# Kernel optimization log

Hardware: AMD Instinct MI355X
Metric: run time of the kernel (lower is better)

## Reference

```python
import jax, jax.numpy as jnp
import numpy as np

FIELD_DIMS = [26000] * 39
EMBED_DIM = 16
MLP_DIMS = [1024, 512, 256]
BATCH = 16384
EPS = 1e-5
OFFSETS = jnp.asarray(np.concatenate(([0], np.cumsum(FIELD_DIMS)[:-1])), dtype=jnp.int64)


def _bn_fields(x, g, b):
    # BatchNorm1d(num_fields) on (B, F, E): stats over (batch, embed) per field (training-mode batch stats)
    mu = x.mean(axis=(0, 2), keepdims=True)
    var = x.var(axis=(0, 2), keepdims=True)
    return (x - mu) / jnp.sqrt(var + EPS) * g[None, :, None] + b[None, :, None]


def _bn1d(x, g, b):
    # BatchNorm1d on (B, D): stats over batch
    mu = x.mean(axis=0)
    var = x.var(axis=0)
    return (x - mu) / jnp.sqrt(var + EPS) * g + b


def setup_inputs() -> dict:
    key = jax.random.key(0)
    ks = jax.random.split(key, 16)
    V = sum(FIELD_DIMS)
    F = len(FIELD_DIMS)
    E = EMBED_DIM
    D = F * E  # 624
    init = lambda k, shape, s: (jax.random.normal(k, shape) * s).astype(jnp.float32)
    inp = {}
    inp["x"] = jax.random.randint(ks[0], (BATCH, F), 0, FIELD_DIMS[0], dtype=jnp.int64)
    inp["emb_table"] = init(ks[1], (V, E), 0.01)
    inp["lin_table"] = init(ks[2], (V, 1), 0.01)
    inp["lin_bias"] = jnp.zeros((1,), jnp.float32)
    inp["bn_g"] = jnp.ones((F,), jnp.float32)
    inp["bn_b"] = jnp.zeros((F,), jnp.float32)
    inp["ctrl_w"] = init(ks[3], (D, F), D ** -0.5)
    inp["ctrl_b"] = jnp.zeros((F,), jnp.float32)
    inp["ctrl_bn_g"] = jnp.ones((F,), jnp.float32)
    inp["ctrl_bn_b"] = jnp.zeros((F,), jnp.float32)
    dims = [D] + MLP_DIMS
    for i in range(3):
        inp[f"w{i+1}"] = init(ks[4 + i], (dims[i], dims[i + 1]), dims[i] ** -0.5)
        inp[f"b{i+1}"] = jnp.zeros((dims[i + 1],), jnp.float32)
        inp[f"g{i+1}"] = jnp.ones((dims[i + 1],), jnp.float32)
        inp[f"be{i+1}"] = jnp.zeros((dims[i + 1],), jnp.float32)
    inp["w_out"] = init(ks[7], (dims[-1], 1), dims[-1] ** -0.5)
    inp["b_out"] = jnp.zeros((1,), jnp.float32)
    inp["k"] = 20
    return inp


def reference(x, emb_table, lin_table, lin_bias, bn_g, bn_b,
              ctrl_w, ctrl_b, ctrl_bn_g, ctrl_bn_b,
              w1, b1, g1, be1, w2, b2, g2, be2, w3, b3, g3, be3,
              w_out, b_out, k):
    B, F = x.shape
    idx = x + OFFSETS[None, :]                      # (B, F) global vocab ids
    embed = emb_table[idx]                          # (B, F, E) gather
    embed = _bn_fields(embed, bn_g, bn_b)
    flat = embed.reshape(B, -1)                     # (B, F*E)
    # controller MLP: Linear -> BN -> ReLU (dropout inactive at inference)
    weight = jax.nn.relu(_bn1d(flat @ ctrl_w + ctrl_b, ctrl_bn_g, ctrl_bn_b))  # (B, F)
    # kmax_pooling along dim 1: topk values, indices sorted ascending
    kvals, kidx = jax.lax.top_k(weight, k)          # (B, k)
    order = jnp.argsort(kidx, axis=1)
    kidx = jnp.take_along_axis(kidx, order, axis=1)
    kvals = jnp.take_along_axis(kvals, order, axis=1)
    kvals = kvals / jnp.sum(kvals, axis=1, keepdims=True)
    # scatter normalized weights into zero mask
    mask = jnp.zeros((B, F), embed.dtype).at[jnp.arange(B)[:, None], kidx].set(kvals)
    embed = embed * mask[:, :, None]                # elementwise gate
    # wide part: sum of per-field scalar embeddings + bias
    linear = lin_table[idx].sum(axis=1) + lin_bias  # (B, 1)
    # deep part: 3-layer MLP with BN+ReLU, final Linear to 1
    h = embed.reshape(B, -1)
    h = jax.nn.relu(_bn1d(h @ w1 + b1, g1, be1))
    h = jax.nn.relu(_bn1d(h @ w2 + b2, g2, be2))
    h = jax.nn.relu(_bn1d(h @ w3 + b3, g3, be3))
    out = linear + h @ w_out + b_out                # (B, 1)
    return jax.nn.sigmoid(out.squeeze(1))           # (B,)
```

## Files before the change

kernel.cpp:

```cpp
#include <hip/hip_runtime.h>
#include <math.h>
#include <stdint.h>

constexpr int BB = 16384;
constexpr int NF = 39;
constexpr int NE = 16;
constexpr int ND = NF * NE;
constexpr int FIELD_DIM = 26000;
constexpr float EPS_ = 1e-5f;

typedef __bf16 bfx8 __attribute__((ext_vector_type(8)));
typedef float f32x4 __attribute__((ext_vector_type(4)));
typedef short s16x8 __attribute__((ext_vector_type(8)));

static __device__ __forceinline__ unsigned short f2bf(float f) {
    union { float f; unsigned u; } a; a.f = f;
    unsigned r = a.u + 0x7fffu + ((a.u >> 16) & 1u);
    return (unsigned short)(r >> 16);
}
static __device__ __forceinline__ float bf2f(unsigned short u) {
    union { unsigned u; float f; } a; a.u = ((unsigned)u) << 16;
    return a.f;
}

static __device__ __forceinline__ void xcd_map(int l, int lognx, int& bx, int& by) {
    int s = l >> 3;
    bx = s & ((1 << lognx) - 1);
    by = ((l & 7) << 4) + (s >> lognx);
}

__global__ void k_prep(const float* __restrict__ w1, const float* __restrict__ w2,
                       const float* __restrict__ w3, const float* __restrict__ cw,
                       unsigned short* __restrict__ w1t, unsigned short* __restrict__ w2t,
                       unsigned short* __restrict__ w3t, float* __restrict__ wct,
                       double* __restrict__ stats, int nstats) {
    int b = blockIdx.x;
    if (b < 1280) {
        const float* in; unsigned short* outp; int K, N, Kpad, tid;
        if (b < 640)        { in = w1; outp = w1t; K = 624;  N = 1024; Kpad = 640;  tid = b; }
        else if (b < 1152)  { in = w2; outp = w2t; K = 1024; N = 512;  Kpad = 1024; tid = b - 640; }
        else                { in = w3; outp = w3t; K = 512;  N = 256;  Kpad = 512;  tid = b - 1152; }
        int tiles_n = N >> 5;
        int tk = tid / tiles_n, tn = tid % tiles_n;
        __shared__ float tile[32][33];
        int tx = threadIdx.x & 31, ty = threadIdx.x >> 5;
#pragma unroll
        for (int i = 0; i < 4; ++i) {
            int k = tk * 32 + ty + i * 8, n = tn * 32 + tx;
            tile[ty + i * 8][tx] = (k < K) ? in[(size_t)k * N + n] : 0.f;
        }
        __syncthreads();
#pragma unroll
        for (int i = 0; i < 4; ++i) {
            int n = tn * 32 + ty + i * 8, k = tk * 32 + tx;
            outp[(size_t)n * Kpad + k] = f2bf(tile[tx][ty + i * 8]);
        }
    } else if (b < 1397) {
        int gid = (b - 1280) * 256 + threadIdx.x;
        if (gid < 48 * ND) {
            int j = gid / ND, k = gid % ND;
            wct[gid] = (j < NF) ? cw[(size_t)k * NF + j] : 0.f;
        }
    } else {
        int gid = (b - 1397) * 256 + threadIdx.x;
        if (gid < nstats) stats[gid] = 0.0;
    }
}

__global__ void k_field_stats(const int* __restrict__ x, const float* __restrict__ emb,
                              double* __restrict__ stats ) {
    int f = blockIdx.x;
    int r = blockIdx.y * blockDim.x + threadIdx.x;
    double s = 0.0, q = 0.0;
    if (r < BB) {
        long long id = (long long)x[r * NF + f] + (long long)f * FIELD_DIM;
        const float4* p = (const float4*)(emb + id * NE);
#pragma unroll
        for (int i = 0; i < 4; ++i) {
            float4 v = p[i];
            s += (double)v.x; s += (double)v.y; s += (double)v.z; s += (double)v.w;
            q += (double)v.x * v.x; q += (double)v.y * v.y;
            q += (double)v.z * v.z; q += (double)v.w * v.w;
        }
    }
    __shared__ double ls[256], lq[256];
    ls[threadIdx.x] = s; lq[threadIdx.x] = q;
    __syncthreads();
    for (int off = 128; off > 0; off >>= 1) {
        if ((int)threadIdx.x < off) {
            ls[threadIdx.x] += ls[threadIdx.x + off];
            lq[threadIdx.x] += lq[threadIdx.x + off];
        }
        __syncthreads();
    }
    if (threadIdx.x == 0) {
        atomicAdd(&stats[f], ls[0]);
        atomicAdd(&stats[NF + f], lq[0]);
    }
}

__global__ void k_flat_norm(const int* __restrict__ x, const float* __restrict__ emb,
                            const double* __restrict__ stats, const float* __restrict__ bng,
                            const float* __restrict__ bnb, float* __restrict__ flat) {
    __shared__ float sc_s[NF], sh_s[NF];
    if ((int)threadIdx.x < NF) {
        int f = threadIdx.x;
        double cnt = (double)BB * NE;
        double mu = stats[f] / cnt;
        double var = stats[NF + f] / cnt - mu * mu;
        float sc = (float)((double)bng[f] / sqrt(var + (double)EPS_));
        sc_s[f] = sc;
        sh_s[f] = bnb[f] - (float)mu * sc;
    }
    __syncthreads();
    int gid = blockIdx.x * blockDim.x + threadIdx.x;
    if (gid >= BB * NF) return;
    int f = gid % NF;
    long long id = (long long)x[gid] + (long long)f * FIELD_DIM;
    float sc = sc_s[f], sh = sh_s[f];
    const float4* p = (const float4*)(emb + id * NE);
    float4* o = (float4*)(flat) + (size_t)gid * 4;
#pragma unroll
    for (int i = 0; i < 4; ++i) {
        float4 v = p[i];
        o[i] = make_float4(fmaf(v.x, sc, sh), fmaf(v.y, sc, sh),
                           fmaf(v.z, sc, sh), fmaf(v.w, sc, sh));
    }
}

__launch_bounds__(256)
__global__ void k_ctrl_gemm_sk(const float* __restrict__ flat, const float* __restrict__ wct,
                               double* __restrict__ zp) {
    __shared__ float As[64][68];
    __shared__ float Ws[64][49];
    const int t = threadIdx.x;
    const int tn = t & 15;
    const int tm = t >> 4;
    const int bm = blockIdx.x & 255;
    const int half = blockIdx.x >> 8;
    const int m0 = bm * 64;
    const int kbeg = half ? 320 : 0;
    const int kend = half ? 624 : 320;
    double acc[4][3] = {};
    for (int k0 = kbeg; k0 < kend; k0 += 64) {
        const int kl = (kend - k0 >= 64) ? 64 : (kend - k0);
        const int kl4 = kl >> 2;
#pragma unroll
        for (int i = 0; i < 4; ++i) {
            int idx = t + 256 * i;
            int row = idx >> 4, c4 = idx & 15;
            if (c4 < kl4) {
                float4 v = *(const float4*)(flat + (size_t)(m0 + row) * ND + k0 + c4 * 4);
                *(float4*)&As[row][c4 * 4] = v;
            }
        }
        {
            int col = t >> 4;
            int c4 = t & 15;
#pragma unroll
            for (int cp = 0; cp < 3; ++cp, col += 16) {
                if (c4 < kl4) {
                    float4 v = *(const float4*)(wct + (size_t)col * ND + k0 + c4 * 4);
                    Ws[c4 * 4 + 0][col] = v.x; Ws[c4 * 4 + 1][col] = v.y;
                    Ws[c4 * 4 + 2][col] = v.z; Ws[c4 * 4 + 3][col] = v.w;
                }
            }
        }
        __syncthreads();
#pragma unroll 4
        for (int kk = 0; kk < kl; ++kk) {
            double a0 = (double)As[4 * tm + 0][kk];
            double a1 = (double)As[4 * tm + 1][kk];
            double a2 = (double)As[4 * tm + 2][kk];
            double a3 = (double)As[4 * tm + 3][kk];
            double w0 = (double)Ws[kk][3 * tn + 0];
            double w1 = (double)Ws[kk][3 * tn + 1];
            double w2 = (double)Ws[kk][3 * tn + 2];
            acc[0][0] += a0 * w0; acc[0][1] += a0 * w1; acc[0][2] += a0 * w2;
            acc[1][0] += a1 * w0; acc[1][1] += a1 * w1; acc[1][2] += a1 * w2;
            acc[2][0] += a2 * w0; acc[2][1] += a2 * w1; acc[2][2] += a2 * w2;
            acc[3][0] += a3 * w0; acc[3][1] += a3 * w1; acc[3][2] += a3 * w2;
        }
        __syncthreads();
    }
    double* zph = zp + (size_t)half * BB * NF;
#pragma unroll
    for (int j = 0; j < 3; ++j) {
        int col = 3 * tn + j;
        if (col < NF) {
#pragma unroll
            for (int i = 0; i < 4; ++i)
                zph[(size_t)(m0 + 4 * tm + i) * NF + col] = acc[i][j];
        }
    }
}

__global__ void k_ctrl_reduce(const double* __restrict__ zp, const float* __restrict__ bias,
                              float* __restrict__ z, double* __restrict__ stats) {
    __shared__ double Sred[2][16][48];
    const int t = threadIdx.x;
    const int tn = t & 15;
    const int tm = t >> 4;
    const int m0 = blockIdx.x * 64;
#pragma unroll
    for (int j = 0; j < 3; ++j) {
        int col = 3 * tn + j;
        double s = 0.0, q = 0.0;
        if (col < NF) {
            float bs = bias[col];
#pragma unroll
            for (int i = 0; i < 4; ++i) {
                size_t idx = (size_t)(m0 + 4 * tm + i) * NF + col;
                double p01 = zp[idx] + zp[(size_t)BB * NF + idx];
                float v = (float)(p01 + (double)bs);
                z[idx] = v;
                s += (double)v;
                q += (double)v * (double)v;
            }
        }
        Sred[0][tm][col] = s;
        Sred[1][tm][col] = q;
    }
    __syncthreads();
    if (t < NF) {
        double ts = 0.0, tq = 0.0;
#pragma unroll
        for (int i = 0; i < 16; ++i) { ts += Sred[0][i][t]; tq += Sred[1][i][t]; }
        atomicAdd(&stats[t], ts);
        atomicAdd(&stats[NF + t], tq);
    }
}

__global__ void k_topk_gate(const float* __restrict__ zc, const double* __restrict__ stats,
                            const float* __restrict__ cbg, const float* __restrict__ cbb,
                            const int* __restrict__ kptr, const float* __restrict__ flat,
                            unsigned short* __restrict__ flatg) {
    __shared__ float sc_s[NF], sh_s[NF];
    int t = threadIdx.x;
    if (t < NF) {
        double mu = stats[t] / (double)BB;
        double var = stats[NF + t] / (double)BB - mu * mu;
        float sc = (float)((double)cbg[t] / sqrt(var + (double)EPS_));
        sc_s[t] = sc;
        sh_s[t] = cbb[t] - (float)mu * sc;
    }
    __syncthreads();
    int r = blockIdx.x * 4 + (t >> 6);
    int lane = t & 63;
    int k = kptr[0];
    bool active = (lane < NF);
    float w = -1.f;
    if (active) {
        float v = zc[(size_t)r * NF + lane];
        w = fmaxf(fmaf(v, sc_s[lane], sh_s[lane]), 0.f);
    }
    int rank = 0;
#pragma unroll
    for (int j = 0; j < NF; ++j) {
        float vj = __shfl(w, j, 64);
        rank += (vj > w || (vj == w && j < lane)) ? 1 : 0;
    }
    bool sel = active && (rank < k);
    float val = sel ? w : 0.f;
    float sum = val;
#pragma unroll
    for (int off = 32; off > 0; off >>= 1) sum += __shfl_xor(sum, off, 64);
    if (active) {
        float ms = sel ? ((sum > 0.f) ? (w / sum) : 0.f) : 0.f;
        const float* src = flat + (size_t)r * ND + lane * 16;
        unsigned short* dst = flatg + (size_t)r * 640 + lane * 16;
#pragma unroll
        for (int h = 0; h < 2; ++h) {
            union { s16x8 v; unsigned short u[8]; } p;
#pragma unroll
            for (int j = 0; j < 8; ++j) p.u[j] = f2bf(src[h * 8 + j] * ms);
            *(s16x8*)(dst + h * 8) = p.v;
        }
    } else if (lane == NF) {
        s16x8 zv = {};
        *(s16x8*)(flatg + (size_t)r * 640 + 624) = zv;
        *(s16x8*)(flatg + (size_t)r * 640 + 632) = zv;
    }
}

__launch_bounds__(256)
__global__ void k_mfma_gemm(const unsigned short* __restrict__ A,
                            const unsigned short* __restrict__ Bt,
                            const float* __restrict__ bias,
                            unsigned short* __restrict__ C,
                            double* __restrict__ stats,
                            int M, int K, int N, int lognx) {
    __shared__ char lds[65536];
    const int t = threadIdx.x;
    const int l = t & 63;
    const int w = t >> 6;
    int bx, by;
    xcd_map(blockIdx.x, lognx, bx, by);
    const int m0 = by * 128, n0 = bx * 128;
    const int Wr = (w >> 1) * 64, Wc = (w & 1) * 64;

    const int srow = t >> 3;
    const int sswz = (t & 7) ^ (srow & 7);
    const unsigned short* ga[4];
    const unsigned short* gb[4];
#pragma unroll
    for (int i = 0; i < 4; ++i) {
        ga[i] = A + (size_t)(m0 + i * 32 + srow) * K + sswz * 8;
        gb[i] = Bt + (size_t)(n0 + i * 32 + srow) * K + sswz * 8;
    }
    int a_off[4][2], b_off[4][2];
#pragma unroll
    for (int m = 0; m < 4; ++m) {
#pragma unroll
        for (int h = 0; h < 2; ++h) {
            int r = Wr + m * 16 + (l & 15);
            a_off[m][h] = r * 128 + (((h * 4 + (l >> 4)) ^ (r & 7)) << 4);
            int c = Wc + m * 16 + (l & 15);
            b_off[m][h] = c * 128 + (((h * 4 + (l >> 4)) ^ (c & 7)) << 4);
        }
    }
    const int nt = K >> 6;
    f32x4 acc[4][4] = {};
#pragma unroll
    for (int i = 0; i < 4; ++i) {
        __builtin_amdgcn_global_load_lds(
            (const __attribute__((address_space(1))) void*)ga[i],
            (__attribute__((address_space(3))) void*)(lds + i * 4096 + t * 16), 16, 0, 0);
        __builtin_amdgcn_global_load_lds(
            (const __attribute__((address_space(1))) void*)gb[i],
            (__attribute__((address_space(3))) void*)(lds + 32768 + i * 4096 + t * 16), 16, 0, 0);
        ga[i] += 64; gb[i] += 64;
    }
    __syncthreads();
    for (int ts = 0; ts < nt; ++ts) {
        const int cur = ts & 1;
        if (ts + 1 < nt) {
            char* An = lds + (cur ^ 1) * 16384;
            char* Bn = lds + 32768 + (cur ^ 1) * 16384;
#pragma unroll
            for (int i = 0; i < 4; ++i) {
                __builtin_amdgcn_global_load_lds(
                    (const __attribute__((address_space(1))) void*)ga[i],
                    (__attribute__((address_space(3))) void*)(An + i * 4096 + t * 16), 16, 0, 0);
                __builtin_amdgcn_global_load_lds(
                    (const __attribute__((address_space(1))) void*)gb[i],
                    (__attribute__((address_space(3))) void*)(Bn + i * 4096 + t * 16), 16, 0, 0);
                ga[i] += 64; gb[i] += 64;
            }
        }
        const char* Ac = lds + cur * 16384;
        const char* Bc = lds + 32768 + cur * 16384;
#pragma unroll
        for (int h = 0; h < 2; ++h) {
            bfx8 af[4], bv[4];
#pragma unroll
            for (int m = 0; m < 4; ++m)
                af[m] = __builtin_bit_cast(bfx8, *(const s16x8*)(Ac + a_off[m][h]));
#pragma unroll
            for (int n = 0; n < 4; ++n)
                bv[n] = __builtin_bit_cast(bfx8, *(const s16x8*)(Bc + b_off[n][h]));
#pragma unroll
            for (int m = 0; m < 4; ++m)
#pragma unroll
                for (int n = 0; n < 4; ++n)
                    acc[m][n] = __builtin_amdgcn_mfma_f32_16x16x32_bf16(af[m], bv[n], acc[m][n], 0, 0, 0);
        }
        __syncthreads();
    }
#pragma unroll
    for (int n = 0; n < 4; ++n) {
        int nc = n0 + Wc + n * 16 + (l & 15);
        float bs = bias[nc];
        double s = 0.0, q = 0.0;
#pragma unroll
        for (int m = 0; m < 4; ++m) {
            int rbase = m0 + Wr + m * 16 + ((l >> 4) << 2);
#pragma unroll
            for (int i = 0; i < 4; ++i) {
                float v = acc[m][n][i] + bs;
                C[(size_t)(rbase + i) * N + nc] = f2bf(v);
                s += (double)v;
                q += (double)v * (double)v;
            }
        }
        s += __shfl_xor(s, 16, 64); s += __shfl_xor(s, 32, 64);
        q += __shfl_xor(q, 16, 64); q += __shfl_xor(q, 32, 64);
        if ((l >> 4) == 0) {
            atomicAdd(&stats[nc], s);
            atomicAdd(&stats[N + nc], q);
        }
    }
}

__launch_bounds__(256)
__global__ void k_mfma_gemm_bn(const unsigned short* __restrict__ A,
                               const double* __restrict__ statsIn,
                               const float* __restrict__ g, const float* __restrict__ be,
                               const unsigned short* __restrict__ Bt,
                               const float* __restrict__ bias,
                               unsigned short* __restrict__ C,
                               double* __restrict__ stats,
                               int M, int K, int N, int lognx) {
    __shared__ char lds[73728];
    float* scs = (float*)(lds + 65536);
    float* shs = scs + K;
    const int t = threadIdx.x;
    const int l = t & 63;
    const int w = t >> 6;
    int bx, by;
    xcd_map(blockIdx.x, lognx, bx, by);
    const int m0 = by * 128, n0 = bx * 128;
    const int Wr = (w >> 1) * 64, Wc = (w & 1) * 64;

    constexpr double inv_bb = 1.0 / (double)BB;
    for (int c = t; c < K; c += 256) {
        double mu = statsIn[c] * inv_bb;
        double var = statsIn[K + c] * inv_bb - mu * mu;
        float sc = g[c] / sqrtf((float)var + EPS_);
        scs[c] = sc;
        shs[c] = be[c] - (float)mu * sc;
    }
    __syncthreads();

    const int srow = t >> 3;
    const int sswz = (t & 7) ^ (srow & 7);
    const unsigned short* ga[4];
    const unsigned short* gb[4];
#pragma unroll
    for (int i = 0; i < 4; ++i) {
        ga[i] = A + (size_t)(m0 + i * 32 + srow) * K + sswz * 8;
        gb[i] = Bt + (size_t)(n0 + i * 32 + srow) * K + sswz * 8;
    }
    int a_off[4][2], b_off[4][2];
#pragma unroll
    for (int m = 0; m < 4; ++m) {
#pragma unroll
        for (int h = 0; h < 2; ++h) {
            int r = Wr + m * 16 + (l & 15);
            a_off[m][h] = r * 128 + (((h * 4 + (l >> 4)) ^ (r & 7)) << 4);
            int c = Wc + m * 16 + (l & 15);
            b_off[m][h] = c * 128 + (((h * 4 + (l >> 4)) ^ (c & 7)) << 4);
        }
    }
    const int nt = K >> 6;
    f32x4 acc[4][4] = {};
    s16x8 praw[4];

    auto write_a = [&](int buf, int kb0) {
        char* Ad = lds + buf * 16384;
        int kb = kb0 + sswz * 8;
        float4 sc0 = *(const float4*)&scs[kb];
        float4 sc1 = *(const float4*)&scs[kb + 4];
        float4 sh0 = *(const float4*)&shs[kb];
        float4 sh1 = *(const float4*)&shs[kb + 4];
        float scl[8] = {sc0.x, sc0.y, sc0.z, sc0.w, sc1.x, sc1.y, sc1.z, sc1.w};
        float shl[8] = {sh0.x, sh0.y, sh0.z, sh0.w, sh1.x, sh1.y, sh1.z, sh1.w};
#pragma unroll
        for (int i = 0; i < 4; ++i) {
            union { s16x8 v; unsigned short u[8]; } pin;
            pin.v = praw[i];
            float f[8];
#pragma unroll
            for (int j = 0; j < 8; ++j)
                f[j] = fmaxf(fmaf(bf2f(pin.u[j]), scl[j], shl[j]), 0.f);
            union { unsigned w4[4]; s16x8 v; } pout;
#pragma unroll
            for (int j = 0; j < 4; ++j) {
                unsigned rr;
                asm("v_cvt_pk_bf16_f32 %0, %1, %2" : "=v"(rr) : "v"(f[2 * j]), "v"(f[2 * j + 1]));
                pout.w4[j] = rr;
            }
            *(s16x8*)(Ad + i * 4096 + t * 16) = pout.v;
        }
    };
    auto load_praw = [&]() {
#pragma unroll
        for (int i = 0; i < 4; ++i) { praw[i] = *(const s16x8*)ga[i]; ga[i] += 64; }
    };
    auto stage_b = [&](int buf) {
        char* Bd = lds + 32768 + buf * 16384;
#pragma unroll
        for (int i = 0; i < 4; ++i) {
            __builtin_amdgcn_global_load_lds(
                (const __attribute__((address_space(1))) void*)gb[i],
                (__attribute__((address_space(3))) void*)(Bd + i * 4096 + t * 16), 16, 0, 0);
            gb[i] += 64;
        }
    };

    load_praw();
    stage_b(0);
    write_a(0, 0);
    if (nt > 1) load_praw();
    __syncthreads();

    for (int ts = 0; ts < nt; ++ts) {
        const int cur = ts & 1;
        if (ts + 1 < nt) {
            stage_b(cur ^ 1);
            write_a(cur ^ 1, (ts + 1) << 6);
            if (ts + 2 < nt) load_praw();
        }
        const char* Ac = lds + cur * 16384;
        const char* Bc = lds + 32768 + cur * 16384;
#pragma unroll
        for (int h = 0; h < 2; ++h) {
            bfx8 af[4], bv[4];
#pragma unroll
            for (int m = 0; m < 4; ++m)
                af[m] = __builtin_bit_cast(bfx8, *(const s16x8*)(Ac + a_off[m][h]));
#pragma unroll
            for (int n = 0; n < 4; ++n)
                bv[n] = __builtin_bit_cast(bfx8, *(const s16x8*)(Bc + b_off[n][h]));
#pragma unroll
            for (int m = 0; m < 4; ++m)
#pragma unroll
                for (int n = 0; n < 4; ++n)
                    acc[m][n] = __builtin_amdgcn_mfma_f32_16x16x32_bf16(af[m], bv[n], acc[m][n], 0, 0, 0);
        }
        __syncthreads();
    }
#pragma unroll
    for (int n = 0; n < 4; ++n) {
        int nc = n0 + Wc + n * 16 + (l & 15);
        float bs = bias[nc];
        double s = 0.0, q = 0.0;
#pragma unroll
        for (int m = 0; m < 4; ++m) {
            int rbase = m0 + Wr + m * 16 + ((l >> 4) << 2);
#pragma unroll
            for (int i = 0; i < 4; ++i) {
                float v = acc[m][n][i] + bs;
                C[(size_t)(rbase + i) * N + nc] = f2bf(v);
                s += (double)v;
                q += (double)v * (double)v;
            }
        }
        s += __shfl_xor(s, 16, 64); s += __shfl_xor(s, 32, 64);
        q += __shfl_xor(q, 16, 64); q += __shfl_xor(q, 32, 64);
        if ((l >> 4) == 0) {
            atomicAdd(&stats[nc], s);
            atomicAdd(&stats[N + nc], q);
        }
    }
}

__global__ void k_out(const unsigned short* __restrict__ h3, const double* __restrict__ stats3,
                      const float* __restrict__ g3, const float* __restrict__ be3,
                      const float* __restrict__ wo, const float* __restrict__ bo,
                      const int* __restrict__ x, const float* __restrict__ lt,
                      const float* __restrict__ lb, float* __restrict__ out) {
    __shared__ float scs[256], shs[256];
    int t = threadIdx.x;
    {
        constexpr double inv_bb = 1.0 / (double)BB;
        double mu = stats3[t] * inv_bb;
        double var = stats3[256 + t] * inv_bb - mu * mu;
        float sc = g3[t] / sqrtf((float)var + EPS_);
        scs[t] = sc;
        shs[t] = be3[t] - (float)mu * sc;
    }
    __syncthreads();
    int r = blockIdx.x * 4 + (t >> 6);
    int lane = t & 63;
    float s = 0.f;
#pragma unroll
    for (int k = lane; k < 256; k += 64) {
        float xv = bf2f(h3[(size_t)r * 256 + k]);
        float hb = bf2f(f2bf(fmaxf(fmaf(xv, scs[k], shs[k]), 0.f)));
        s += hb * wo[k];
    }
    if (lane < NF) {
        long long id = (long long)x[r * NF + lane] + (long long)lane * FIELD_DIM;
        s += lt[id];
    }
#pragma unroll
    for (int off = 32; off > 0; off >>= 1) s += __shfl_xor(s, off, 64);
    if (lane == 0) {
        float tt = s + bo[0] + lb[0];
        out[r] = 1.f / (1.f + expf(-tt));
    }
}

extern "C" void kernel_launch(void* const* d_in, const int* in_sizes, int n_in,
                              void* d_out, int out_size, void* d_ws, size_t ws_size,
                              hipStream_t stream) {
    const int* x = (const int*)d_in[0];
    const float* emb = (const float*)d_in[1];
    const float* lint = (const float*)d_in[2];
    const float* linb = (const float*)d_in[3];
    const float* bng = (const float*)d_in[4];
    const float* bnb = (const float*)d_in[5];
    const float* cw = (const float*)d_in[6];
    const float* cb = (const float*)d_in[7];
    const float* cbg = (const float*)d_in[8];
    const float* cbb = (const float*)d_in[9];
    const float* w1 = (const float*)d_in[10];
    const float* b1 = (const float*)d_in[11];
    const float* g1 = (const float*)d_in[12];
    const float* be1 = (const float*)d_in[13];
    const float* w2 = (const float*)d_in[14];
    const float* b2 = (const float*)d_in[15];
    const float* g2 = (const float*)d_in[16];
    const float* be2 = (const float*)d_in[17];
    const float* w3 = (const float*)d_in[18];
    const float* b3 = (const float*)d_in[19];
    const float* g3 = (const float*)d_in[20];
    const float* be3 = (const float*)d_in[21];
    const float* wo = (const float*)d_in[22];
    const float* bo = (const float*)d_in[23];
    const int* kptr = (const int*)d_in[24];
    float* out = (float*)d_out;

    char* p = (char*)d_ws;
    float* flat = (float*)p;                 p += (size_t)BB * ND * 4;
    unsigned short* flatg = (unsigned short*)p; p += (size_t)BB * 640 * 2;
    unsigned short* h1 = (unsigned short*)p; p += (size_t)BB * 1024 * 2;
    unsigned short* h2 = (unsigned short*)p; p += (size_t)BB * 512 * 2;
    unsigned short* h3 = (unsigned short*)p; p += (size_t)BB * 256 * 2;
    unsigned short* w1t = (unsigned short*)p; p += (size_t)1024 * 640 * 2;
    unsigned short* w2t = (unsigned short*)p; p += (size_t)512 * 1024 * 2;
    unsigned short* w3t = (unsigned short*)p; p += (size_t)256 * 512 * 2;
    float* wct = (float*)p;                  p += (size_t)48 * ND * 4;
    float* zc = (float*)p;                   p += (size_t)BB * NF * 4;
    double* zp = (double*)p;                 p += (size_t)2 * BB * NF * 8;
    double* stats_all = (double*)p;
    double* stats_f = stats_all;
    double* stats_c = stats_f + 2 * NF;
    double* stats_1 = stats_c + 2 * NF;
    double* stats_2 = stats_1 + 2 * 1024;
    double* stats_3 = stats_2 + 2 * 512;
    int stats_doubles = 2 * (NF + NF + 1024 + 512 + 256);

    k_prep<<<1412, 256, 0, stream>>>(w1, w2, w3, cw, w1t, w2t, w3t, wct,
                                     stats_all, stats_doubles);

    k_field_stats<<<dim3(NF, BB / 256), 256, 0, stream>>>(x, emb, stats_f);
    k_flat_norm<<<(BB * NF + 255) / 256, 256, 0, stream>>>(x, emb, stats_f, bng, bnb, flat);

    k_ctrl_gemm_sk<<<512, 256, 0, stream>>>(flat, wct, zp);
    k_ctrl_reduce<<<BB / 64, 256, 0, stream>>>(zp, cb, zc, stats_c);
    k_topk_gate<<<BB / 4, 256, 0, stream>>>(zc, stats_c, cbg, cbb, kptr, flat, flatg);

    k_mfma_gemm<<<(1024 / 128) * (BB / 128), 256, 0, stream>>>(flatg, w1t, b1, h1, stats_1,
                                                               BB, 640, 1024, 3);

    k_mfma_gemm_bn<<<(512 / 128) * (BB / 128), 256, 0, stream>>>(h1, stats_1, g1, be1,
                                                                 w2t, b2, h2, stats_2,
                                                                 BB, 1024, 512, 2);

    k_mfma_gemm_bn<<<(256 / 128) * (BB / 128), 256, 0, stream>>>(h2, stats_2, g2, be2,
                                                                 w3t, b3, h3, stats_3,
                                                                 BB, 512, 256, 1);

    k_out<<<BB / 4, 256, 0, stream>>>(h3, stats_3, g3, be3, wo, bo, x, lint, linb, out);
}
```

Measured before the change: 224.1 us.

## Fuse field-BN embedding gather into controller GEMM and top-k gate kernels

Removes the k_flat_norm kernel and its 40MB fp32 'flat' intermediate. The controller GEMM now gathers embedding rows directly through per-block index offsets in shared memory and applies the field batch-norm scale and shift while loading A tiles. The top-k gate kernel likewise re-gathers and normalizes the embeddings itself. The cost is extra random gathers from the embedding table (twice, plus the stats pass) and repeated BN coefficient computation per block, in exchange for saving one kernel launch and a full write plus two reads of the flat buffer.

```diff
diff --git a/kernel.cpp b/kernel.cpp
--- a/kernel.cpp
+++ b/kernel.cpp
@@ -99,40 +99,15 @@
     }
 }
 
-__global__ void k_flat_norm(const int* __restrict__ x, const float* __restrict__ emb,
-                            const double* __restrict__ stats, const float* __restrict__ bng,
-                            const float* __restrict__ bnb, float* __restrict__ flat) {
-    __shared__ float sc_s[NF], sh_s[NF];
-    if ((int)threadIdx.x < NF) {
-        int f = threadIdx.x;
-        double cnt = (double)BB * NE;
-        double mu = stats[f] / cnt;
-        double var = stats[NF + f] / cnt - mu * mu;
-        float sc = (float)((double)bng[f] / sqrt(var + (double)EPS_));
-        sc_s[f] = sc;
-        sh_s[f] = bnb[f] - (float)mu * sc;
-    }
-    __syncthreads();
-    int gid = blockIdx.x * blockDim.x + threadIdx.x;
-    if (gid >= BB * NF) return;
-    int f = gid % NF;
-    long long id = (long long)x[gid] + (long long)f * FIELD_DIM;
-    float sc = sc_s[f], sh = sh_s[f];
-    const float4* p = (const float4*)(emb + id * NE);
-    float4* o = (float4*)(flat) + (size_t)gid * 4;
-#pragma unroll
-    for (int i = 0; i < 4; ++i) {
-        float4 v = p[i];
-        o[i] = make_float4(fmaf(v.x, sc, sh), fmaf(v.y, sc, sh),
-                           fmaf(v.z, sc, sh), fmaf(v.w, sc, sh));
-    }
-}
-
 __launch_bounds__(256)
-__global__ void k_ctrl_gemm_sk(const float* __restrict__ flat, const float* __restrict__ wct,
-                               double* __restrict__ zp) {
+__global__ void k_ctrl_gemm_sk(const int* __restrict__ x, const float* __restrict__ emb,
+                               const double* __restrict__ stats_f,
+                               const float* __restrict__ bng, const float* __restrict__ bnb,
+                               const float* __restrict__ wct, double* __restrict__ zp) {
     __shared__ float As[64][68];
     __shared__ float Ws[64][49];
+    __shared__ int xoff[64 * NF];
+    __shared__ float fsc[NF], fsh[NF];
     const int t = threadIdx.x;
     const int tn = t & 15;
     const int tm = t >> 4;
@@ -141,6 +116,22 @@
     const int m0 = bm * 64;
     const int kbeg = half ? 320 : 0;
     const int kend = half ? 624 : 320;
+
+    if (t < NF) {
+        double cnt = (double)BB * NE;
+        double mu = stats_f[t] / cnt;
+        double var = stats_f[NF + t] / cnt - mu * mu;
+        float sc = (float)((double)bng[t] / sqrt(var + (double)EPS_));
+        fsc[t] = sc;
+        fsh[t] = bnb[t] - (float)mu * sc;
+    }
+    const int* xrow = x + m0 * NF;
+    for (int j = t; j < 64 * NF; j += 256) {
+        int f = j % NF;
+        xoff[j] = (xrow[j] + f * FIELD_DIM) * NE;
+    }
+    __syncthreads();
+
     double acc[4][3] = {};
     for (int k0 = kbeg; k0 < kend; k0 += 64) {
         const int kl = (kend - k0 >= 64) ? 64 : (kend - k0);
@@ -150,8 +141,13 @@
             int idx = t + 256 * i;
             int row = idx >> 4, c4 = idx & 15;
             if (c4 < kl4) {
-                float4 v = *(const float4*)(flat + (size_t)(m0 + row) * ND + k0 + c4 * 4);
-                *(float4*)&As[row][c4 * 4] = v;
+                int k = k0 + c4 * 4;
+                int f = k >> 4;
+                float4 v = *(const float4*)(emb + xoff[row * NF + f] + (k & 12));
+                float sc = fsc[f], sh = fsh[f];
+                float4 nv = make_float4(fmaf(v.x, sc, sh), fmaf(v.y, sc, sh),
+                                        fmaf(v.z, sc, sh), fmaf(v.w, sc, sh));
+                *(float4*)&As[row][c4 * 4] = nv;
             }
         }
         {
@@ -233,9 +229,11 @@
 
 __global__ void k_topk_gate(const float* __restrict__ zc, const double* __restrict__ stats,
                             const float* __restrict__ cbg, const float* __restrict__ cbb,
-                            const int* __restrict__ kptr, const float* __restrict__ flat,
+                            const int* __restrict__ kptr, const int* __restrict__ x,
+                            const float* __restrict__ emb, const double* __restrict__ stats_f,
+                            const float* __restrict__ bng, const float* __restrict__ bnb,
                             unsigned short* __restrict__ flatg) {
-    __shared__ float sc_s[NF], sh_s[NF];
+    __shared__ float sc_s[NF], sh_s[NF], fsc[NF], fsh[NF];
     int t = threadIdx.x;
     if (t < NF) {
         double mu = stats[t] / (double)BB;
@@ -243,6 +241,12 @@
         float sc = (float)((double)cbg[t] / sqrt(var + (double)EPS_));
         sc_s[t] = sc;
         sh_s[t] = cbb[t] - (float)mu * sc;
+        double cnt = (double)BB * NE;
+        double muf = stats_f[t] / cnt;
+        double varf = stats_f[NF + t] / cnt - muf * muf;
+        float scf = (float)((double)bng[t] / sqrt(varf + (double)EPS_));
+        fsc[t] = scf;
+        fsh[t] = bnb[t] - (float)muf * scf;
     }
     __syncthreads();
     int r = blockIdx.x * 4 + (t >> 6);
@@ -267,13 +271,18 @@
     for (int off = 32; off > 0; off >>= 1) sum += __shfl_xor(sum, off, 64);
     if (active) {
         float ms = sel ? ((sum > 0.f) ? (w / sum) : 0.f) : 0.f;
-        const float* src = flat + (size_t)r * ND + lane * 16;
+        int o = (x[r * NF + lane] + lane * FIELD_DIM) * NE;
+        const float4* pe = (const float4*)(emb + o);
+        float sc = fsc[lane], sh = fsh[lane];
         unsigned short* dst = flatg + (size_t)r * 640 + lane * 16;
 #pragma unroll
         for (int h = 0; h < 2; ++h) {
+            float4 e0 = pe[h * 2], e1 = pe[h * 2 + 1];
+            float e[8] = {e0.x, e0.y, e0.z, e0.w, e1.x, e1.y, e1.z, e1.w};
             union { s16x8 v; unsigned short u[8]; } p;
 #pragma unroll
-            for (int j = 0; j < 8; ++j) p.u[j] = f2bf(src[h * 8 + j] * ms);
+            for (int j = 0; j < 8; ++j)
+                p.u[j] = f2bf(fmaf(e[j], sc, sh) * ms);
             *(s16x8*)(dst + h * 8) = p.v;
         }
     } else if (lane == NF) {
@@ -613,7 +622,6 @@
     float* out = (float*)d_out;
 
     char* p = (char*)d_ws;
-    float* flat = (float*)p;                 p += (size_t)BB * ND * 4;
     unsigned short* flatg = (unsigned short*)p; p += (size_t)BB * 640 * 2;
     unsigned short* h1 = (unsigned short*)p; p += (size_t)BB * 1024 * 2;
     unsigned short* h2 = (unsigned short*)p; p += (size_t)BB * 512 * 2;
@@ -636,11 +644,11 @@
                                      stats_all, stats_doubles);
 
     k_field_stats<<<dim3(NF, BB / 256), 256, 0, stream>>>(x, emb, stats_f);
-    k_flat_norm<<<(BB * NF + 255) / 256, 256, 0, stream>>>(x, emb, stats_f, bng, bnb, flat);
-
-    k_ctrl_gemm_sk<<<512, 256, 0, stream>>>(flat, wct, zp);
+
+    k_ctrl_gemm_sk<<<512, 256, 0, stream>>>(x, emb, stats_f, bng, bnb, wct, zp);
     k_ctrl_reduce<<<BB / 64, 256, 0, stream>>>(zp, cb, zc, stats_c);
-    k_topk_gate<<<BB / 4, 256, 0, stream>>>(zc, stats_c, cbg, cbb, kptr, flat, flatg);
+    k_topk_gate<<<BB / 4, 256, 0, stream>>>(zc, stats_c, cbg, cbb, kptr, x, emb,
+                                            stats_f, bng, bnb, flatg);
 
     k_mfma_gemm<<<(1024 / 128) * (BB / 128), 256, 0, stream>>>(flatg, w1t, b1, h1, stats_1,
                                                                BB, 640, 1024, 3);
```

After: 211.0 us. -5.8%, faster.
